# Kernel tuning notes

Measured on AMD Instinct MI355X. Metric: run time of the kernel, lower is better.

Reference implementation:

```python
import jax, jax.numpy as jnp
import numpy as np
from jax import lax

N_SAMPLES = 2 ** 15          # 32768
N_FRAMES = 128
N_HARMONICS = 8
FILT_SIZE = 64
N_EVENTS = 8
N_SCALE = 128                # len(MusicalScale()) assumed = 128 (MIDI notes)
NYQ = 11025.0                # SR22050 nyquist
MIN_F0 = 40.0 / NYQ
MAX_F0 = 3000.0 / NYQ
F0_SPAN = MAX_F0 - MIN_F0
MIN_RES = 0.9
RES_SPAN = 1.0 - MIN_RES
PI = float(np.pi)

# packed layout slices (order of param_sizes dict)
SL_F0 = slice(0, 128)
SL_FINE = slice(128, 256)
SL_AMP = slice(256, 384)
SL_HAMP = slice(384, 392)
SL_HDEC = slice(392, 400)
SL_FENV = slice(400, 464)


def lin_interp(x, out_size):
    """F.interpolate(mode='linear', align_corners=False) along last axis."""
    n = x.shape[-1]
    pos = (jnp.arange(out_size, dtype=x.dtype) + 0.5) * (n / out_size) - 0.5
    pos = jnp.clip(pos, 0.0, n - 1)
    lo = jnp.floor(pos).astype(jnp.int32)
    hi = jnp.minimum(lo + 1, n - 1)
    w = pos - lo.astype(x.dtype)
    return x[..., lo] * (1.0 - w) + x[..., hi] * w


def setup_inputs() -> dict:
    key = jax.random.key(0)
    k1, k2 = jax.random.split(key)
    B = 32 * N_EVENTS  # 256 event rows
    packed = jax.random.normal(k1, (B, 464), dtype=jnp.float32)
    # musical scale: MIDI-note center frequencies normalized by nyquist
    midi = np.arange(N_SCALE)
    freqs = 440.0 * 2.0 ** ((midi - 69) / 12.0) / NYQ
    frequencies = jnp.asarray(freqs, dtype=jnp.float32)
    noise = jax.random.uniform(k2, (B, 1, N_SAMPLES), dtype=jnp.float32)  # mapped to (-1,1) in reference
    return {"packed": packed, "frequencies": frequencies, "noise": noise}


def reference(packed, frequencies, noise):
    B = packed.shape[0]
    p = jax.nn.sigmoid(packed)  # Model applies activation(p) before SynthParams

    # f0: softmax over discrete scale bins, weighted sum of normalized freqs
    f0w = jax.nn.softmax(p[:, SL_F0], axis=-1)             # [B, 128]
    f0 = (f0w @ frequencies)[:, None, None]                # [B,1,1]
    f0 = jnp.broadcast_to(f0, (B, 1, N_FRAMES))            # repeat over frames
    f0 = f0 * NYQ
    f0 = MIN_F0 + f0 * F0_SPAN                             # [B,1,128]
    # NOTE: source computes `f0 + f0 + f0_fine` and discards it -> f0_fine unused

    harmonic_factors = jnp.arange(1, N_HARMONICS + 1, dtype=p.dtype)
    osc = f0 * harmonic_factors[None, :, None]             # [B,8,128]
    radians = osc / NYQ * PI
    radians = lin_interp(radians, N_SAMPLES)               # [B,8,32768]
    osc_bank = jnp.sin(jnp.cumsum(radians, axis=-1))

    harm_decay = MIN_RES + p[:, SL_HDEC] * RES_SPAN        # [B,8]
    harm_amp = p[:, SL_HAMP]                               # [B,8]
    amp = p[:, SL_AMP][:, None, :] * 2.0 - 1.0             # [B,1,128]
    amp_full = lin_interp(amp, N_SAMPLES)                  # [B,1,32768]

    noise_filter = p[:, SL_FENV][:, None, :]               # [B,1,64]
    noise_filter = lin_interp(noise_filter, N_SAMPLES // 2)
    noise_filter = jnp.pad(noise_filter, ((0, 0), (0, 0), (0, 1)))  # [B,1,16385]

    noise_u = noise * 2.0 - 1.0                            # uniform(-1,1)
    noise_spec = jnp.fft.rfft(noise_u, axis=-1, norm='ortho')
    filt = jnp.fft.irfft(noise_spec * noise_filter, n=N_SAMPLES, axis=-1, norm='ortho')
    filt = filt * jnp.clip(amp_full, 0.0, 1.0)             # [B,1,32768]

    # leaky-accumulator recurrence over frames
    def step(cur, a_i):  # cur [B,8], a_i [B]
        cur = jnp.clip(cur + a_i[:, None] * harm_amp, 0.0, 1.0)
        out = cur
        cur = cur * harm_decay
        return cur, out

    amp_t = amp[:, 0, :].T                                 # [128, B]
    _, outs = lax.scan(step, jnp.zeros((B, N_HARMONICS), dtype=p.dtype), amp_t)
    x = jnp.transpose(outs, (1, 2, 0))                     # [B,8,128]
    x = jnp.where(x >= PI, 0.0, x)
    x = lin_interp(x, N_SAMPLES)                           # [B,8,32768]
    x = x * osc_bank
    x = filt + x
    x = x.reshape(-1, N_EVENTS, N_HARMONICS, N_SAMPLES)
    x = jnp.sum(x, axis=(1, 2))[:, None, :]                # [batch,1,32768]
    return x
```

## Files before the change

### kernel.cpp

```cpp
#include <hip/hip_runtime.h>
#include <math.h>

#ifndef M_PI
#define M_PI 3.14159265358979323846
#endif

#define NSAMP 32768
#define MHALF 16384
#define TWO_PI_F 6.2831853071795864f
#define PSTRIDE 1089

typedef float v2 __attribute__((ext_vector_type(2)));

__device__ __forceinline__ double dsig(double x) { return 1.0 / (1.0 + exp(-x)); }

__device__ __forceinline__ v2 cmul(v2 a, v2 b) {
    return a.xx * b + (v2){-a.y, a.y} * b.yx;
}

template<int INV>
__device__ __forceinline__ void fft4(v2& x0, v2& x1, v2& x2, v2& x3) {
    v2 s02 = x0 + x2;
    v2 d02 = x0 - x2;
    v2 s13 = x1 + x3;
    v2 d13 = x1 - x3;
    v2 j13 = INV ? (v2){-d13.y, d13.x} : (v2){d13.y, -d13.x};
    x0 = s02 + s13;
    x2 = s02 - s13;
    x1 = d02 + j13;
    x3 = d02 - j13;
}

#define V16(v, c) v[((((c) & 3) << 2) | ((c) >> 2))]

template<int INV>
__device__ __forceinline__ void fft16(v2 v[16]) {
    const float s = INV ? 1.0f : -1.0f;
#pragma unroll
    for (int b = 0; b < 4; b++) fft4<INV>(v[b], v[4 + b], v[8 + b], v[12 + b]);
    v[5]  = cmul(v[5],  (v2){0.9238795325f,  s * 0.3826834324f});
    v[9]  = cmul(v[9],  (v2){0.7071067812f,  s * 0.7071067812f});
    v[13] = cmul(v[13], (v2){0.3826834324f,  s * 0.9238795325f});
    v[6]  = cmul(v[6],  (v2){0.7071067812f,  s * 0.7071067812f});
    v[10] = cmul(v[10], (v2){0.0f,           s * 1.0f});
    v[14] = cmul(v[14], (v2){-0.7071067812f, s * 0.7071067812f});
    v[7]  = cmul(v[7],  (v2){0.3826834324f,  s * 0.9238795325f});
    v[11] = cmul(v[11], (v2){-0.7071067812f, s * 0.7071067812f});
    v[15] = cmul(v[15], (v2){-0.9238795325f, s * -0.3826834324f});
#pragma unroll
    for (int p = 0; p < 4; p++) fft4<INV>(v[4 * p], v[4 * p + 1], v[4 * p + 2], v[4 * p + 3]);
}

__device__ __forceinline__ int zaddr(int k) {
    int p = k & 15, k2 = k >> 4;
    int s = 256 * (k2 & 3) + 16 * ((k2 >> 2) & 15) + (k2 >> 6);
    return p * PSTRIDE + s + (s >> 4);
}

__device__ __forceinline__ void plane_fwd(v2* __restrict__ Zp, int l) {
    {
        float sn, cs;
        __sincosf(TWO_PI_F * (float)l * (1.f / 1024.f), &sn, &cs);
        v2 w1 = (v2){cs, -sn};
        const v2 jstep = (v2){0.9238795325f, -0.3826834324f};
#pragma unroll
        for (int j = 0; j < 4; j++) {
            const int r = 64 * j + l;
            v2 u0 = Zp[r], u1 = Zp[256 + r], u2 = Zp[512 + r], u3 = Zp[768 + r];
            fft4<0>(u0, u1, u2, u3);
            v2 w2 = cmul(w1, w1);
            v2 w3 = cmul(w2, w1);
            Zp[r] = u0;
            Zp[256 + r] = cmul(u1, w1);
            Zp[512 + r] = cmul(u2, w2);
            Zp[768 + r] = cmul(u3, w3);
            w1 = cmul(w1, jstep);
        }
    }
    {
        const int k4 = l >> 4, c = l & 15;
        const int nbase = 256 * k4 + c;
        float sn, cs;
        __sincosf(TWO_PI_F * (float)c * (1.f / 256.f), &sn, &cs);
        const v2 wc = (v2){cs, -sn};
        v2 v[16];
#pragma unroll
        for (int b = 0; b < 16; b++) v[b] = Zp[nbase + 16 * b];
        fft16<0>(v);
        const int pbase = 272 * k4 + c;
        Zp[pbase] = V16(v, 0);
        v2 w = wc;
#pragma unroll
        for (int kb = 1; kb < 16; kb++) {
            Zp[pbase + 17 * kb] = cmul(V16(v, kb), w);
            w = cmul(w, wc);
        }
    }
    {
        const int pbase = 272 * (l >> 4) + 17 * (l & 15);
        v2 v[16];
#pragma unroll
        for (int c = 0; c < 16; c++) v[c] = Zp[pbase + c];
        fft16<0>(v);
#pragma unroll
        for (int kc = 0; kc < 16; kc++) Zp[pbase + kc] = V16(v, kc);
    }
}

__device__ __forceinline__ void plane_inv(v2* __restrict__ Zp, int l) {
    {
        const int kb = l & 15;
        const int pbase = 272 * (l >> 4) + 17 * kb;
        float sn, cs;
        __sincosf(TWO_PI_F * (float)kb * (1.f / 256.f), &sn, &cs);
        const v2 wkb = (v2){cs, sn};
        v2 v[16];
#pragma unroll
        for (int kc = 0; kc < 16; kc++) v[kc] = Zp[pbase + kc];
        fft16<1>(v);
        Zp[pbase] = V16(v, 0);
        v2 w = wkb;
#pragma unroll
        for (int nc = 1; nc < 16; nc++) {
            Zp[pbase + nc] = cmul(V16(v, nc), w);
            w = cmul(w, wkb);
        }
    }
    {
        const int k4 = l >> 4, nc = l & 15;
        const int pbase = 272 * k4 + nc;
        float sni, csi;
        __sincosf(TWO_PI_F * (float)(nc * k4) * (1.f / 1024.f), &sni, &csi);
        v2 t = (v2){csi, sni};
        float sns, css;
        __sincosf(TWO_PI_F * (float)k4 * (1.f / 64.f), &sns, &css);
        const v2 st = (v2){css, sns};
        v2 v[16];
#pragma unroll
        for (int kb = 0; kb < 16; kb++) v[kb] = Zp[pbase + 17 * kb];
        fft16<1>(v);
#pragma unroll
        for (int nb = 0; nb < 16; nb++) {
            Zp[pbase + 17 * nb] = cmul(V16(v, nb), t);
            t = cmul(t, st);
        }
    }
#pragma unroll
    for (int j = 0; j < 4; j++) {
        const int r = 64 * j + l;
        const int rp = r + (r >> 4);
        v2 u0 = Zp[rp], u1 = Zp[272 + rp], u2 = Zp[544 + rp], u3 = Zp[816 + rp];
        fft4<1>(u0, u1, u2, u3);
        Zp[rp] = u0; Zp[272 + rp] = u1; Zp[544 + rp] = u2; Zp[816 + rp] = u3;
    }
}

__device__ __forceinline__ float hinterp64(const float* f, int j) {
    float pos = ((float)j + 0.5f) * (1.0f / 256.0f) - 0.5f;
    pos = fminf(fmaxf(pos, 0.0f), 63.0f);
    int lo = (int)pos;
    int hi = min(lo + 1, 63);
    float w = pos - (float)lo;
    return f[lo] * (1.0f - w) + f[hi] * w;
}

__global__ __launch_bounds__(1024, 4) void fft_kernel(
    const float* __restrict__ packed, const float* __restrict__ freqs,
    const float* __restrict__ noise,
    unsigned long long* __restrict__ step, float* __restrict__ env,
    float* __restrict__ filt)
{
    __shared__ v2 Z[16 * PSTRIDE];
    __shared__ float fenv_s[64];
    __shared__ float amp_s[128];
    __shared__ double ampd_s[128];
    const int bb = blockIdx.x;
    const int tid = threadIdx.x;
    const int wv = tid >> 6, l = tid & 63;

    if (tid < 64) {
        const float* pk = packed + bb * 464;
        double e0 = exp(dsig((double)pk[tid]));
        double e1 = exp(dsig((double)pk[tid + 64]));
        double num = e0 * (double)freqs[tid] + e1 * (double)freqs[tid + 64];
        double den = e0 + e1;
#pragma unroll
        for (int off = 32; off > 0; off >>= 1) {
            num += __shfl_down(num, off);
            den += __shfl_down(den, off);
        }
        num = __shfl(num, 0);
        den = __shfl(den, 0);

        double a0 = dsig((double)pk[256 + tid]) * 2.0 - 1.0;
        double a1 = dsig((double)pk[256 + 64 + tid]) * 2.0 - 1.0;
        ampd_s[tid] = a0; ampd_s[tid + 64] = a1;
        amp_s[tid] = (float)a0; amp_s[tid + 64] = (float)a1;
        fenv_s[tid] = (float)dsig((double)pk[400 + tid]);

        if (tid < 8) {
            const double NYQ = 11025.0;
            const double MIN_F0 = 40.0 / NYQ;
            const double MAX_F0 = 3000.0 / NYQ;
            const double F0_SPAN = MAX_F0 - MIN_F0;
            double f0 = num / den;
            double F = f0 * NYQ;
            double G = MIN_F0 + F * F0_SPAN;
            double oscf = G * (double)(tid + 1);
            double r = oscf / NYQ * M_PI;
            double rv = r / (2.0 * M_PI);
            rv -= floor(rv);
            step[bb * 8 + tid] = (unsigned long long)(rv * 18446744073709551616.0);

            double ha = dsig((double)pk[384 + tid]);
            double hd = 0.9 + dsig((double)pk[392 + tid]) * (1.0 - 0.9);
            double cur = 0.0;
            float* eo = env + (size_t)(bb * 8 + tid) * 128;
            for (int fr = 0; fr < 128; fr++) {
                cur = cur + ampd_s[fr] * ha;
                cur = fmin(fmax(cur, 0.0), 1.0);
                eo[fr] = (float)cur;
                cur *= hd;
            }
        }
    }

    const v2* nz = (const v2*)(noise + (size_t)bb * NSAMP);

    {
        v2 v[16];
#pragma unroll
        for (int a = 0; a < 16; a++) {
            v2 t = nz[a * 1024 + tid];
            v[a] = t * 2.f - 1.f;
        }
        fft16<0>(v);
        float sn, cs;
        __sincosf(TWO_PI_F * (float)tid * (1.f / 16384.f), &sn, &cs);
        const v2 ws = (v2){cs, -sn};
        Z[tid] = V16(v, 0);
        v2 w = ws;
#pragma unroll
        for (int k1 = 1; k1 < 16; k1++) {
            Z[k1 * PSTRIDE + tid] = cmul(V16(v, k1), w);
            w = cmul(w, ws);
        }
    }
    __syncthreads();

    plane_fwd(Z + wv * PSTRIDE, l);
    __syncthreads();

    const float invM = 1.0f / (float)MHALF;
    {
        float sn0, cs0;
        __sincosf((float)M_PI * (float)tid * (1.f / 16384.f), &sn0, &cs0);
        v2 t = (v2){cs0, sn0};
        const v2 tstep = (v2){0.98078528040323f, 0.19509032201613f};
        for (int k = tid; k <= 8192; k += 1024) {
            if (k == 0) {
                int i0 = zaddr(0);
                v2 Z0 = Z[i0];
                float Y0 = (Z0.x + Z0.y) * hinterp64(fenv_s, 0);
                float vv = Y0 * 0.5f * invM;
                Z[i0] = (v2){vv, vv};
            } else if (k == 8192) {
                int i8 = zaddr(8192);
                float s = hinterp64(fenv_s, 8192) * invM;
                Z[i8] = Z[i8] * s;
            } else {
                int ik = zaddr(k), imk = zaddr(16384 - k);
                v2 Zk = Z[ik], Zm = Z[imk];
                float Ex = 0.5f * (Zk.x + Zm.x);
                float Ey = 0.5f * (Zk.y - Zm.y);
                float Ox = 0.5f * (Zk.y + Zm.y);
                float Oy = -0.5f * (Zk.x - Zm.x);
                float cs = t.x, sn = t.y;
                float Xkx = Ex + cs * Ox + sn * Oy;
                float Xky = Ey + cs * Oy - sn * Ox;
                float Xmx = Ex - cs * Ox - sn * Oy;
                float Xmy = -Ey + cs * Oy - sn * Ox;
                float Hk = hinterp64(fenv_s, k);
                float Hm = hinterp64(fenv_s, 16384 - k);
                float Ykx = Xkx * Hk, Yky = Xky * Hk;
                float Ymx = Xmx * Hm, Ymy = Xmy * Hm;
                float Er = 0.5f * (Ykx + Ymx);
                float Ei = 0.5f * (Yky - Ymy);
                float Pr = 0.5f * (Ykx - Ymx);
                float Pi = 0.5f * (Yky + Ymy);
                float Oyx = Pr * cs - Pi * sn;
                float Oyy = Pr * sn + Pi * cs;
                Z[ik]  = (v2){(Er - Oyy) * invM, (Ei + Oyx) * invM};
                Z[imk] = (v2){(Er + Oyy) * invM, (-Ei + Oyx) * invM};
            }
            t = cmul(t, tstep);
        }
    }
    __syncthreads();

    plane_inv(Z + wv * PSTRIDE, l);
    __syncthreads();

    {
        const int tp = tid + (tid >> 4);
        v2 v[16];
#pragma unroll
        for (int k1 = 0; k1 < 16; k1++) v[k1] = Z[k1 * PSTRIDE + tp];
        float sn, cs;
        __sincosf(TWO_PI_F * (float)tid * (1.f / 16384.f), &sn, &cs);
        const v2 wg = (v2){cs, sn};
        v2 w = wg;
#pragma unroll
        for (int k1 = 1; k1 < 16; k1++) {
            v[k1] = cmul(v[k1], w);
            w = cmul(w, wg);
        }
        fft16<1>(v);

        v2* fo = (v2*)(filt + (size_t)bb * NSAMP);
#pragma unroll
        for (int m = 0; m < 16; m++) {
            v2 y = V16(v, m);
            int A = m * 1024 + tid;
            int s0 = 2 * A;
            float p0 = ((float)s0 + 0.5f) * (1.0f / 256.0f) - 0.5f;
            float p1 = p0 + (1.0f / 256.0f);
            p0 = fminf(fmaxf(p0, 0.0f), 127.0f);
            p1 = fminf(fmaxf(p1, 0.0f), 127.0f);
            int l0 = (int)p0, l1 = (int)p1;
            int h0 = min(l0 + 1, 127), h1 = min(l1 + 1, 127);
            float w0a = p0 - (float)l0, w1a = p1 - (float)l1;
            float a0 = amp_s[l0] * (1.0f - w0a) + amp_s[h0] * w0a;
            float a1 = amp_s[l1] * (1.0f - w1a) + amp_s[h1] * w1a;
            a0 = fminf(fmaxf(a0, 0.0f), 1.0f);
            a1 = fminf(fmaxf(a1, 0.0f), 1.0f);
            fo[A] = (v2){y.x * a0, y.y * a1};
        }
    }
}

__global__ __launch_bounds__(256) void synth_kernel(
    const unsigned long long* __restrict__ step, const float* __restrict__ env,
    const float* __restrict__ filt, float* __restrict__ out)
{
    const int chunk = blockIdx.x;
    const int g = blockIdx.y;
    const int tid = threadIdx.x;
    __shared__ float env_s[64 * 128];
    __shared__ unsigned long long step_s[64];

    const float* eg = env + (size_t)g * 64 * 128;
    for (int i = tid; i < 64 * 128; i += 256) env_s[i] = eg[i];
    if (tid < 64) step_s[tid] = step[g * 64 + tid];
    __syncthreads();

    const int s0 = chunk * 1024 + tid * 4;

    float4 aF = make_float4(0.f, 0.f, 0.f, 0.f);
#pragma unroll
    for (int e = 0; e < 8; e++) {
        const float4 f = *(const float4*)(filt + ((size_t)(g * 8 + e)) * NSAMP + s0);
        aF.x += f.x; aF.y += f.y; aF.z += f.z; aF.w += f.w;
    }

    float c0v[4], c1v[4], c2v[4];
    int lo0;
    {
        float pos0 = ((float)s0 + 0.5f) * (1.0f / 256.0f) - 0.5f;
        pos0 = fminf(fmaxf(pos0, 0.0f), 127.0f);
        lo0 = (int)pos0;
#pragma unroll
        for (int k = 0; k < 4; k++) {
            float pos = ((float)(s0 + k) + 0.5f) * (1.0f / 256.0f) - 0.5f;
            pos = fminf(fmaxf(pos, 0.0f), 127.0f);
            int lo = (int)pos;
            float w = pos - (float)lo;
            if (lo == lo0) { c0v[k] = 1.0f - w; c1v[k] = w;        c2v[k] = 0.0f; }
            else           { c0v[k] = 0.0f;     c1v[k] = 1.0f - w; c2v[k] = w;    }
        }
    }
    const int i1 = min(lo0 + 1, 127);
    int lo3b = lo0;
    {
        float pos = ((float)(s0 + 3) + 0.5f) * (1.0f / 256.0f) - 0.5f;
        pos = fminf(fmaxf(pos, 0.0f), 127.0f);
        lo3b = (int)pos;
    }
    const int i2 = min(lo3b + 1, 127);

    float a0 = 0.f, a1 = 0.f, a2 = 0.f, a3 = 0.f;
    const unsigned long long n0 = (unsigned long long)(unsigned)(s0 + 1);

#pragma unroll 8
    for (int idx = 0; idx < 64; idx++) {
        const unsigned long long st = step_s[idx];
        const unsigned long long p = st * n0;
        const float stf = (float)(unsigned)(st >> 32) * 0x1p-32f;
        float fr = (float)(unsigned)(p >> 32) * 0x1p-32f;
        const float* er = env_s + (idx << 7);
        const float v0 = er[lo0], v1 = er[i1], v2 = er[i2];

        float ev, sn;

        sn = __builtin_amdgcn_sinf(fr);
        ev = fmaf(v0, c0v[0], fmaf(v1, c1v[0], v2 * c2v[0]));
        a0 = fmaf(ev, sn, a0);
        fr = __builtin_amdgcn_fractf(fr + stf);

        sn = __builtin_amdgcn_sinf(fr);
        ev = fmaf(v0, c0v[1], fmaf(v1, c1v[1], v2 * c2v[1]));
        a1 = fmaf(ev, sn, a1);
        fr = __builtin_amdgcn_fractf(fr + stf);

        sn = __builtin_amdgcn_sinf(fr);
        ev = fmaf(v0, c0v[2], fmaf(v1, c1v[2], v2 * c2v[2]));
        a2 = fmaf(ev, sn, a2);
        fr = __builtin_amdgcn_fractf(fr + stf);

        sn = __builtin_amdgcn_sinf(fr);
        ev = fmaf(v0, c0v[3], fmaf(v1, c1v[3], v2 * c2v[3]));
        a3 = fmaf(ev, sn, a3);
    }

    float4 r;
    r.x = a0 + 8.0f * aF.x;
    r.y = a1 + 8.0f * aF.y;
    r.z = a2 + 8.0f * aF.z;
    r.w = a3 + 8.0f * aF.w;
    *(float4*)(out + (size_t)g * NSAMP + s0) = r;
}

extern "C" void kernel_launch(void* const* d_in, const int* in_sizes, int n_in,
                              void* d_out, int out_size, void* d_ws, size_t ws_size,
                              hipStream_t stream)
{
    (void)in_sizes; (void)n_in; (void)out_size; (void)ws_size;
    const float* packed = (const float*)d_in[0];
    const float* freqs  = (const float*)d_in[1];
    const float* noise  = (const float*)d_in[2];
    float* out = (float*)d_out;
    char* ws = (char*)d_ws;

    unsigned long long* step = (unsigned long long*)(ws);
    float* env  = (float*)(ws + 16384);
    float* filt = (float*)(ws + 16384 + 1048576 + 131072 + 65536);

    hipLaunchKernelGGL(fft_kernel, dim3(256), dim3(1024), 0, stream,
                       packed, freqs, noise, step, env, filt);
    hipLaunchKernelGGL(synth_kernel, dim3(32, 32), dim3(256), 0, stream,
                       step, env, filt, out);
}
```

Measured before the change: 123.4 us.

## Fuse FFT noise filter and harmonic synthesis into one kernel with atomic accumulation

Merges the FFT/filter kernel and the synth kernel into a single kernel, one block per event row. The filtered noise and the per-event envelopes and steps stay in shared memory instead of passing through the global workspace. Each block adds its event's contribution into the output with float atomics, after a memset that zeroes the output. This removes the workspace write and read-back and one kernel launch. In exchange it adds eight-way atomic contention per output sample, makes float summation order nondeterministic, and keeps only 256 large blocks on the device.

```diff
diff --git a/kernel.cpp b/kernel.cpp
--- a/kernel.cpp
+++ b/kernel.cpp
@@ -164,17 +164,20 @@
     return f[lo] * (1.0f - w) + f[hi] * w;
 }
 
-__global__ __launch_bounds__(1024, 4) void fft_kernel(
+__global__ __launch_bounds__(1024, 4) void fused_kernel(
     const float* __restrict__ packed, const float* __restrict__ freqs,
-    const float* __restrict__ noise,
-    unsigned long long* __restrict__ step, float* __restrict__ env,
-    float* __restrict__ filt)
+    const float* __restrict__ noise, float* __restrict__ out)
 {
     __shared__ v2 Z[16 * PSTRIDE];
     __shared__ float fenv_s[64];
     __shared__ float amp_s[128];
     __shared__ double ampd_s[128];
-    const int bb = blockIdx.x;
+    __shared__ float env_s[8 * 128];
+    __shared__ unsigned long long step_s[8];
+
+    const int bid = blockIdx.x;
+    const int g = bid & 31;
+    const int bb = g * 8 + (bid >> 5);
     const int tid = threadIdx.x;
     const int wv = tid >> 6, l = tid & 63;
 
@@ -210,12 +213,12 @@
             double r = oscf / NYQ * M_PI;
             double rv = r / (2.0 * M_PI);
             rv -= floor(rv);
-            step[bb * 8 + tid] = (unsigned long long)(rv * 18446744073709551616.0);
+            step_s[tid] = (unsigned long long)(rv * 18446744073709551616.0);
 
             double ha = dsig((double)pk[384 + tid]);
             double hd = 0.9 + dsig((double)pk[392 + tid]) * (1.0 - 0.9);
             double cur = 0.0;
-            float* eo = env + (size_t)(bb * 8 + tid) * 128;
+            float* eo = env_s + (tid << 7);
             for (int fr = 0; fr < 128; fr++) {
                 cur = cur + ampd_s[fr] * ha;
                 cur = fmin(fmax(cur, 0.0), 1.0);
@@ -301,11 +304,14 @@
     plane_inv(Z + wv * PSTRIDE, l);
     __syncthreads();
 
+    v2 v[16];
     {
         const int tp = tid + (tid >> 4);
-        v2 v[16];
 #pragma unroll
         for (int k1 = 0; k1 < 16; k1++) v[k1] = Z[k1 * PSTRIDE + tp];
+    }
+    __syncthreads();
+    {
         float sn, cs;
         __sincosf(TWO_PI_F * (float)tid * (1.f / 16384.f), &sn, &cs);
         const v2 wg = (v2){cs, sn};
@@ -317,7 +323,7 @@
         }
         fft16<1>(v);
 
-        v2* fo = (v2*)(filt + (size_t)bb * NSAMP);
+        float* Zf = (float*)Z;
 #pragma unroll
         for (int m = 0; m < 16; m++) {
             v2 y = V16(v, m);
@@ -334,119 +340,100 @@
             float a1 = amp_s[l1] * (1.0f - w1a) + amp_s[h1] * w1a;
             a0 = fminf(fmaxf(a0, 0.0f), 1.0f);
             a1 = fminf(fmaxf(a1, 0.0f), 1.0f);
-            fo[A] = (v2){y.x * a0, y.y * a1};
-        }
-    }
-}
-
-__global__ __launch_bounds__(256) void synth_kernel(
-    const unsigned long long* __restrict__ step, const float* __restrict__ env,
-    const float* __restrict__ filt, float* __restrict__ out)
-{
-    const int chunk = blockIdx.x;
-    const int g = blockIdx.y;
-    const int tid = threadIdx.x;
-    __shared__ float env_s[64 * 128];
-    __shared__ unsigned long long step_s[64];
-
-    const float* eg = env + (size_t)g * 64 * 128;
-    for (int i = tid; i < 64 * 128; i += 256) env_s[i] = eg[i];
-    if (tid < 64) step_s[tid] = step[g * 64 + tid];
-    __syncthreads();
-
-    const int s0 = chunk * 1024 + tid * 4;
-
-    float4 aF = make_float4(0.f, 0.f, 0.f, 0.f);
-#pragma unroll
-    for (int e = 0; e < 8; e++) {
-        const float4 f = *(const float4*)(filt + ((size_t)(g * 8 + e)) * NSAMP + s0);
-        aF.x += f.x; aF.y += f.y; aF.z += f.z; aF.w += f.w;
-    }
-
-    float c0v[4], c1v[4], c2v[4];
-    int lo0;
-    {
-        float pos0 = ((float)s0 + 0.5f) * (1.0f / 256.0f) - 0.5f;
-        pos0 = fminf(fmaxf(pos0, 0.0f), 127.0f);
-        lo0 = (int)pos0;
-#pragma unroll
-        for (int k = 0; k < 4; k++) {
-            float pos = ((float)(s0 + k) + 0.5f) * (1.0f / 256.0f) - 0.5f;
-            pos = fminf(fmaxf(pos, 0.0f), 127.0f);
-            int lo = (int)pos;
-            float w = pos - (float)lo;
-            if (lo == lo0) { c0v[k] = 1.0f - w; c1v[k] = w;        c2v[k] = 0.0f; }
-            else           { c0v[k] = 0.0f;     c1v[k] = 1.0f - w; c2v[k] = w;    }
-        }
-    }
-    const int i1 = min(lo0 + 1, 127);
-    int lo3b = lo0;
-    {
-        float pos = ((float)(s0 + 3) + 0.5f) * (1.0f / 256.0f) - 0.5f;
-        pos = fminf(fmaxf(pos, 0.0f), 127.0f);
-        lo3b = (int)pos;
-    }
-    const int i2 = min(lo3b + 1, 127);
-
-    float a0 = 0.f, a1 = 0.f, a2 = 0.f, a3 = 0.f;
-    const unsigned long long n0 = (unsigned long long)(unsigned)(s0 + 1);
-
-#pragma unroll 8
-    for (int idx = 0; idx < 64; idx++) {
-        const unsigned long long st = step_s[idx];
-        const unsigned long long p = st * n0;
-        const float stf = (float)(unsigned)(st >> 32) * 0x1p-32f;
-        float fr = (float)(unsigned)(p >> 32) * 0x1p-32f;
-        const float* er = env_s + (idx << 7);
-        const float v0 = er[lo0], v1 = er[i1], v2 = er[i2];
-
-        float ev, sn;
-
-        sn = __builtin_amdgcn_sinf(fr);
-        ev = fmaf(v0, c0v[0], fmaf(v1, c1v[0], v2 * c2v[0]));
-        a0 = fmaf(ev, sn, a0);
-        fr = __builtin_amdgcn_fractf(fr + stf);
-
-        sn = __builtin_amdgcn_sinf(fr);
-        ev = fmaf(v0, c0v[1], fmaf(v1, c1v[1], v2 * c2v[1]));
-        a1 = fmaf(ev, sn, a1);
-        fr = __builtin_amdgcn_fractf(fr + stf);
-
-        sn = __builtin_amdgcn_sinf(fr);
-        ev = fmaf(v0, c0v[2], fmaf(v1, c1v[2], v2 * c2v[2]));
-        a2 = fmaf(ev, sn, a2);
-        fr = __builtin_amdgcn_fractf(fr + stf);
-
-        sn = __builtin_amdgcn_sinf(fr);
-        ev = fmaf(v0, c0v[3], fmaf(v1, c1v[3], v2 * c2v[3]));
-        a3 = fmaf(ev, sn, a3);
-    }
-
-    float4 r;
-    r.x = a0 + 8.0f * aF.x;
-    r.y = a1 + 8.0f * aF.y;
-    r.z = a2 + 8.0f * aF.z;
-    r.w = a3 + 8.0f * aF.w;
-    *(float4*)(out + (size_t)g * NSAMP + s0) = r;
+            int d = s0 + 2 * (A >> 5);
+            *(v2*)(Zf + d) = (v2){8.0f * y.x * a0, 8.0f * y.y * a1};
+        }
+    }
+    __syncthreads();
+
+    {
+        const float* Zf = (const float*)Z;
+        float* og = out + (size_t)g * NSAMP;
+#pragma unroll 1
+        for (int j = 0; j < 8; j++) {
+            const int s0 = (tid << 2) + (j << 12);
+
+            float c0v[4], c1v[4], c2v[4];
+            int lo0;
+            {
+                float pos0 = ((float)s0 + 0.5f) * (1.0f / 256.0f) - 0.5f;
+                pos0 = fminf(fmaxf(pos0, 0.0f), 127.0f);
+                lo0 = (int)pos0;
+#pragma unroll
+                for (int k = 0; k < 4; k++) {
+                    float pos = ((float)(s0 + k) + 0.5f) * (1.0f / 256.0f) - 0.5f;
+                    pos = fminf(fmaxf(pos, 0.0f), 127.0f);
+                    int lo = (int)pos;
+                    float w = pos - (float)lo;
+                    if (lo == lo0) { c0v[k] = 1.0f - w; c1v[k] = w;        c2v[k] = 0.0f; }
+                    else           { c0v[k] = 0.0f;     c1v[k] = 1.0f - w; c2v[k] = w;    }
+                }
+            }
+            const int i1 = min(lo0 + 1, 127);
+            int lo3b;
+            {
+                float pos = ((float)(s0 + 3) + 0.5f) * (1.0f / 256.0f) - 0.5f;
+                pos = fminf(fmaxf(pos, 0.0f), 127.0f);
+                lo3b = (int)pos;
+            }
+            const int i2 = min(lo3b + 1, 127);
+
+            const int d0 = s0 + 2 * (s0 >> 6);
+            v2 f01 = *(const v2*)(Zf + d0);
+            v2 f23 = *(const v2*)(Zf + d0 + 2);
+            float a0 = f01.x, a1 = f01.y, a2 = f23.x, a3 = f23.y;
+            const unsigned long long n0 = (unsigned long long)(unsigned)(s0 + 1);
+
+#pragma unroll
+            for (int h = 0; h < 8; h++) {
+                const unsigned long long st = step_s[h];
+                const unsigned long long pp = st * n0;
+                const float stf = (float)(unsigned)(st >> 32) * 0x1p-32f;
+                float fr = (float)(unsigned)(pp >> 32) * 0x1p-32f;
+                const float* er = env_s + (h << 7);
+                const float v0 = er[lo0], v1 = er[i1], ve2 = er[i2];
+
+                float ev, sn;
+
+                sn = __builtin_amdgcn_sinf(fr);
+                ev = fmaf(v0, c0v[0], fmaf(v1, c1v[0], ve2 * c2v[0]));
+                a0 = fmaf(ev, sn, a0);
+                fr = __builtin_amdgcn_fractf(fr + stf);
+
+                sn = __builtin_amdgcn_sinf(fr);
+                ev = fmaf(v0, c0v[1], fmaf(v1, c1v[1], ve2 * c2v[1]));
+                a1 = fmaf(ev, sn, a1);
+                fr = __builtin_amdgcn_fractf(fr + stf);
+
+                sn = __builtin_amdgcn_sinf(fr);
+                ev = fmaf(v0, c0v[2], fmaf(v1, c1v[2], ve2 * c2v[2]));
+                a2 = fmaf(ev, sn, a2);
+                fr = __builtin_amdgcn_fractf(fr + stf);
+
+                sn = __builtin_amdgcn_sinf(fr);
+                ev = fmaf(v0, c0v[3], fmaf(v1, c1v[3], ve2 * c2v[3]));
+                a3 = fmaf(ev, sn, a3);
+            }
+
+            unsafeAtomicAdd(og + s0,     a0);
+            unsafeAtomicAdd(og + s0 + 1, a1);
+            unsafeAtomicAdd(og + s0 + 2, a2);
+            unsafeAtomicAdd(og + s0 + 3, a3);
+        }
+    }
 }
 
 extern "C" void kernel_launch(void* const* d_in, const int* in_sizes, int n_in,
                               void* d_out, int out_size, void* d_ws, size_t ws_size,
                               hipStream_t stream)
 {
-    (void)in_sizes; (void)n_in; (void)out_size; (void)ws_size;
+    (void)in_sizes; (void)n_in; (void)d_ws; (void)ws_size;
     const float* packed = (const float*)d_in[0];
     const float* freqs  = (const float*)d_in[1];
     const float* noise  = (const float*)d_in[2];
     float* out = (float*)d_out;
-    char* ws = (char*)d_ws;
-
-    unsigned long long* step = (unsigned long long*)(ws);
-    float* env  = (float*)(ws + 16384);
-    float* filt = (float*)(ws + 16384 + 1048576 + 131072 + 65536);
-
-    hipLaunchKernelGGL(fft_kernel, dim3(256), dim3(1024), 0, stream,
-                       packed, freqs, noise, step, env, filt);
-    hipLaunchKernelGGL(synth_kernel, dim3(32, 32), dim3(256), 0, stream,
-                       step, env, filt, out);
-}
+
+    hipMemsetAsync(d_out, 0, (size_t)out_size, stream);
+    hipLaunchKernelGGL(fused_kernel, dim3(256), dim3(1024), 0, stream,
+                       packed, freqs, noise, out);
+}
```

After: 202.7 us. 1.64x slower.
